# Optimization experiments

Measured on AMD Instinct MI355X. Metric: run time of the kernel, lower is better.

The kernel has to match this reference:

```python
import jax, jax.numpy as jnp
import numpy as np

H = 16      # num_heads
D = 1024    # hidden_dim
HD = D // H # head_dim = 64


def setup_inputs() -> dict:
    key = jax.random.key(0)
    ks = jax.random.split(key, 9)
    s = 1.0 / np.sqrt(D)
    return {
        "hidden_states": jax.random.normal(ks[0], (2, 2048, D), dtype=jnp.float32),
        "wq": jax.random.uniform(ks[1], (D, D), jnp.float32, -s, s),
        "bq": jax.random.uniform(ks[2], (D,), jnp.float32, -s, s),
        "wk": jax.random.uniform(ks[3], (D, D), jnp.float32, -s, s),
        "bk": jax.random.uniform(ks[4], (D,), jnp.float32, -s, s),
        "wv": jax.random.uniform(ks[5], (D, D), jnp.float32, -s, s),
        "bv": jax.random.uniform(ks[6], (D,), jnp.float32, -s, s),
        "wo": jax.random.uniform(ks[7], (D, D), jnp.float32, -s, s),
        "bo": jax.random.uniform(ks[8], (D,), jnp.float32, -s, s),
    }


def reference(hidden_states, wq, bq, wk, bk, wv, bv, wo, bo):
    B, L, _ = hidden_states.shape
    scale = HD ** -0.5
    # projections: [B,L,D] -> [B,H,L,HD]
    def split_heads(x):
        return x.reshape(B, L, H, HD).transpose(0, 2, 1, 3)
    q = split_heads(hidden_states @ wq.T + bq)
    k = split_heads(hidden_states @ wk.T + bk)
    v = split_heads(hidden_states @ wv.T + bv)
    # explicit [B,H,L,L] scores + softmax + weighted sum (faithful to source)
    scores = jnp.einsum("bhqd,bhkd->bhqk", q, k) * scale
    attn = jax.nn.softmax(scores, axis=-1)
    out = jnp.einsum("bhqk,bhkd->bhqd", attn, v)
    out = out.transpose(0, 2, 1, 3).reshape(B, L, D)
    return out @ wo.T + bo
```

## Files before the change

kernel.cpp:

```cpp
#include <hip/hip_runtime.h>
#include <math.h>

#define BATCH  2
#define SEQ    2048
#define NH     16
#define DMODEL 1024
#define DHEAD  64

typedef short short8 __attribute__((ext_vector_type(8)));
typedef float f32x4 __attribute__((ext_vector_type(4)));

#define QSCALE 0.18033688011112042f

__device__ __forceinline__ ushort f2bf(float f) {
  unsigned int u = __builtin_bit_cast(unsigned int, f);
  u = (u + 0x7FFFu + ((u >> 16) & 1u)) >> 16;
  return (ushort)u;
}

__global__ __launch_bounds__(256) void cast_all(
    const float* __restrict__ hs, const float* __restrict__ wq,
    const float* __restrict__ wk, const float* __restrict__ wv,
    const float* __restrict__ wo,
    ushort* __restrict__ hsb, ushort* __restrict__ wqb,
    ushort* __restrict__ wkb, ushort* __restrict__ wvb,
    ushort* __restrict__ wob) {
  const int z = blockIdx.y;
  const float* s = (z == 0) ? hs : (z == 1) ? wq : (z == 2) ? wk
                   : (z == 3) ? wv : wo;
  ushort* d = (z == 0) ? hsb : (z == 1) ? wqb : (z == 2) ? wkb
              : (z == 3) ? wvb : wob;
  const int n = (z == 0) ? BATCH * SEQ * DMODEL : DMODEL * DMODEL;
  const int i = (blockIdx.x * 256 + threadIdx.x) * 8;
  if (i < n) {
    const float4 a = *(const float4*)(s + i);
    const float4 b = *(const float4*)(s + i + 4);
    short8 o;
    o[0] = (short)f2bf(a.x); o[1] = (short)f2bf(a.y);
    o[2] = (short)f2bf(a.z); o[3] = (short)f2bf(a.w);
    o[4] = (short)f2bf(b.x); o[5] = (short)f2bf(b.y);
    o[6] = (short)f2bf(b.z); o[7] = (short)f2bf(b.w);
    *(short8*)(d + i) = o;
  }
}

__device__ __forceinline__ void mfma_gemm_core(
    const ushort* __restrict__ X, const ushort* __restrict__ W,
    f32x4 (&acc)[4][2]) {
  __shared__ ushort Al[128][40];
  __shared__ ushort Bl[128][40];
  const int tid = threadIdx.x;
  const int lane = tid & 63;
  const int w8 = tid >> 6;
  const int wm = w8 >> 2;
  const int wn = w8 & 3;
  const int m16 = lane & 15;
  const int g4 = lane >> 4;
  const int m0 = blockIdx.y << 7;
  const int n0 = blockIdx.x << 7;

  const int srow = tid >> 2;
  const int sseg = (tid & 3) << 3;
  const ushort* ap = X + (size_t)(m0 + srow) * DMODEL + sseg;
  const ushort* wp = W + (size_t)(n0 + srow) * DMODEL + sseg;

  short8 pa = *(const short8*)(ap);
  short8 pb = *(const short8*)(wp);

  for (int kt = 0; kt < DMODEL / 32; ++kt) {
    __syncthreads();
    *(short8*)&Al[srow][sseg] = pa;
    *(short8*)&Bl[srow][sseg] = pb;
    __syncthreads();
    if (kt < DMODEL / 32 - 1) {
      pa = *(const short8*)(ap + (kt + 1) * 32);
      pb = *(const short8*)(wp + (kt + 1) * 32);
    }
    short8 af[4], bf[2];
#pragma unroll
    for (int mi = 0; mi < 4; ++mi)
      af[mi] = *(const short8*)&Al[(wm << 6) + (mi << 4) + m16][g4 << 3];
#pragma unroll
    for (int ni = 0; ni < 2; ++ni)
      bf[ni] = *(const short8*)&Bl[(wn << 5) + (ni << 4) + m16][g4 << 3];
#pragma unroll
    for (int mi = 0; mi < 4; ++mi)
#pragma unroll
      for (int ni = 0; ni < 2; ++ni)
        acc[mi][ni] = __builtin_amdgcn_mfma_f32_16x16x32_bf16(
            af[mi], bf[ni], acc[mi][ni], 0, 0, 0);
  }
}

__global__ __launch_bounds__(512) void qkv_mfma(
    const ushort* __restrict__ X,
    const ushort* __restrict__ wqb, const ushort* __restrict__ wkb,
    const ushort* __restrict__ wvb,
    const float* __restrict__ bq, const float* __restrict__ bk,
    const float* __restrict__ bv,
    ushort* __restrict__ Qb, ushort* __restrict__ Kb,
    ushort* __restrict__ Vb) {
  const int z = blockIdx.z;
  const ushort* W = (z == 0) ? wqb : (z == 1) ? wkb : wvb;
  const float* bias = (z == 0) ? bq : (z == 1) ? bk : bv;
  ushort* Y = (z == 0) ? Qb : (z == 1) ? Kb : Vb;
  const float oscale = (z == 0) ? QSCALE : 1.0f;

  f32x4 acc[4][2];
#pragma unroll
  for (int mi = 0; mi < 4; ++mi)
#pragma unroll
    for (int ni = 0; ni < 2; ++ni) acc[mi][ni] = (f32x4){0.f, 0.f, 0.f, 0.f};
  mfma_gemm_core(X, W, acc);

  const int tid = threadIdx.x;
  const int lane = tid & 63;
  const int w8 = tid >> 6;
  const int wm = w8 >> 2, wn = w8 & 3;
  const int m16 = lane & 15, g4 = lane >> 4;
  const int m0 = blockIdx.y << 7, n0 = blockIdx.x << 7;
#pragma unroll
  for (int ni = 0; ni < 2; ++ni) {
    const int col = n0 + (wn << 5) + (ni << 4) + m16;
    const float bv4 = bias[col];
#pragma unroll
    for (int mi = 0; mi < 4; ++mi)
#pragma unroll
      for (int r = 0; r < 4; ++r) {
        const int row = m0 + (wm << 6) + (mi << 4) + (g4 << 2) + r;
        Y[(size_t)row * DMODEL + col] = f2bf((acc[mi][ni][r] + bv4) * oscale);
      }
  }
}

__global__ __launch_bounds__(512) void oproj_mfma(
    const ushort* __restrict__ X, const ushort* __restrict__ wob,
    const float* __restrict__ bo, float* __restrict__ Y) {
  f32x4 acc[4][2];
#pragma unroll
  for (int mi = 0; mi < 4; ++mi)
#pragma unroll
    for (int ni = 0; ni < 2; ++ni) acc[mi][ni] = (f32x4){0.f, 0.f, 0.f, 0.f};
  mfma_gemm_core(X, wob, acc);

  const int tid = threadIdx.x;
  const int lane = tid & 63;
  const int w8 = tid >> 6;
  const int wm = w8 >> 2, wn = w8 & 3;
  const int m16 = lane & 15, g4 = lane >> 4;
  const int m0 = blockIdx.y << 7, n0 = blockIdx.x << 7;
#pragma unroll
  for (int ni = 0; ni < 2; ++ni) {
    const int col = n0 + (wn << 5) + (ni << 4) + m16;
    const float bv4 = bo[col];
#pragma unroll
    for (int mi = 0; mi < 4; ++mi)
#pragma unroll
      for (int r = 0; r < 4; ++r) {
        const int row = m0 + (wm << 6) + (mi << 4) + (g4 << 2) + r;
        Y[(size_t)row * DMODEL + col] = acc[mi][ni][r] + bv4;
      }
  }
}

__global__ __launch_bounds__(512, 4) void attn_mfma(
    const ushort* __restrict__ Q, const ushort* __restrict__ K,
    const ushort* __restrict__ V, ushort* __restrict__ O) {
  __shared__ ushort Klds[2][64][72];
  __shared__ ushort Vlds[2][64][72];
  __shared__ ushort Plds[8][16][72];

  const int tid = threadIdx.x;
  const int lane = tid & 63;
  const int wv = tid >> 6;
  const int m16 = lane & 15;
  const int g4 = lane >> 4;
  const int b = blockIdx.z;
  const int h = blockIdx.y;
  const int q0 = (blockIdx.x << 7) + (wv << 4);

  const size_t base = ((size_t)b * SEQ) * DMODEL + h * DHEAD;

  short8 qf[2];
  {
    const ushort* qp = Q + base + (size_t)(q0 + m16) * DMODEL + (g4 << 3);
    qf[0] = *(const short8*)(qp);
    qf[1] = *(const short8*)(qp + 32);
  }

  f32x4 oacc[4];
#pragma unroll
  for (int dt = 0; dt < 4; ++dt) oacc[dt] = (f32x4){0.f, 0.f, 0.f, 0.f};
  float mrow = -1e30f;
  float lsum = 0.f;

  const int skey = tid >> 3;
  const int sseg = tid & 7;
  const ushort* kgp = K + base + (size_t)skey * DMODEL + (sseg << 3);
  const ushort* vgp = V + base + (size_t)skey * DMODEL + (sseg << 3);
  const int vswz_key = skey ^ (sseg << 3);

  short8 kvec = *(const short8*)(kgp);
  short8 vvec = *(const short8*)(vgp);

  int p = 0;
  for (int kt = 0; kt < SEQ / 64; ++kt) {
    *(short8*)&Klds[p][skey][sseg << 3] = kvec;
#pragma unroll
    for (int i = 0; i < 8; ++i)
      Vlds[p][(sseg << 3) + i][vswz_key] = ((const ushort*)&vvec)[i];
    __syncthreads();
    if (kt + 1 < SEQ / 64) {
      const size_t koff = (size_t)(kt + 1) * 64 * DMODEL;
      kvec = *(const short8*)(kgp + koff);
      vvec = *(const short8*)(vgp + koff);
    }

    f32x4 s[4];
#pragma unroll
    for (int kt2 = 0; kt2 < 4; ++kt2) s[kt2] = (f32x4){0.f, 0.f, 0.f, 0.f};
    __builtin_amdgcn_s_setprio(1);
#pragma unroll
    for (int ks = 0; ks < 2; ++ks) {
#pragma unroll
      for (int kt2 = 0; kt2 < 4; ++kt2) {
        const short8 kf =
            *(const short8*)&Klds[p][(kt2 << 4) + m16][(ks << 5) + (g4 << 3)];
        s[kt2] =
            __builtin_amdgcn_mfma_f32_16x16x32_bf16(kf, qf[ks], s[kt2], 0, 0, 0);
      }
    }
    __builtin_amdgcn_s_setprio(0);

    float t01 = fmaxf(fmaxf(s[0][0], s[0][1]), fmaxf(s[0][2], s[0][3]));
    float t11 = fmaxf(fmaxf(s[1][0], s[1][1]), fmaxf(s[1][2], s[1][3]));
    float t21 = fmaxf(fmaxf(s[2][0], s[2][1]), fmaxf(s[2][2], s[2][3]));
    float t31 = fmaxf(fmaxf(s[3][0], s[3][1]), fmaxf(s[3][2], s[3][3]));
    float tred = fmaxf(fmaxf(t01, t11), fmaxf(t21, t31));
    tred = fmaxf(tred, __shfl_xor(tred, 16));
    tred = fmaxf(tred, __shfl_xor(tred, 32));
    if (!__all(tred <= mrow + 8.0f)) {
      const float mnew = fmaxf(mrow, tred);
      const float corr = exp2f(mrow - mnew);
      lsum *= corr;
      const float cb0 = __shfl(corr, (g4 << 2) + 0);
      const float cb1 = __shfl(corr, (g4 << 2) + 1);
      const float cb2 = __shfl(corr, (g4 << 2) + 2);
      const float cb3 = __shfl(corr, (g4 << 2) + 3);
#pragma unroll
      for (int dt = 0; dt < 4; ++dt) {
        oacc[dt][0] *= cb0; oacc[dt][1] *= cb1;
        oacc[dt][2] *= cb2; oacc[dt][3] *= cb3;
      }
      mrow = mnew;
    }
    float ps = 0.f;
#pragma unroll
    for (int kt2 = 0; kt2 < 4; ++kt2)
#pragma unroll
      for (int r = 0; r < 4; ++r) {
        const float pv = exp2f(s[kt2][r] - mrow);
        s[kt2][r] = pv;
        ps += pv;
      }
    lsum += ps;

#pragma unroll
    for (int kt2 = 0; kt2 < 4; ++kt2) {
      const uint lo = (uint)f2bf(s[kt2][0]) | ((uint)f2bf(s[kt2][1]) << 16);
      const uint hi = (uint)f2bf(s[kt2][2]) | ((uint)f2bf(s[kt2][3]) << 16);
      uint2* dst = (uint2*)&Plds[wv][m16][(kt2 << 4) + (g4 << 2)];
      *dst = make_uint2(lo, hi);
    }

    short8 pf[2];
#pragma unroll
    for (int ks = 0; ks < 2; ++ks)
      pf[ks] = *(const short8*)&Plds[wv][m16][(ks << 5) + (g4 << 3)];
    __builtin_amdgcn_s_setprio(1);
#pragma unroll
    for (int dt = 0; dt < 4; ++dt) {
      const int d = (dt << 4) + m16;
      const int swz = (d >> 3) << 3;
#pragma unroll
      for (int ks = 0; ks < 2; ++ks) {
        const short8 vf =
            *(const short8*)&Vlds[p][d][((ks << 5) + (g4 << 3)) ^ swz];
        oacc[dt] =
            __builtin_amdgcn_mfma_f32_16x16x32_bf16(pf[ks], vf, oacc[dt], 0, 0, 0);
      }
    }
    __builtin_amdgcn_s_setprio(0);
    p ^= 1;
  }

  lsum += __shfl_xor(lsum, 16);
  lsum += __shfl_xor(lsum, 32);
  const float inv = 1.0f / lsum;
  const float inv0 = __shfl(inv, (g4 << 2) + 0);
  const float inv1 = __shfl(inv, (g4 << 2) + 1);
  const float inv2 = __shfl(inv, (g4 << 2) + 2);
  const float inv3 = __shfl(inv, (g4 << 2) + 3);
  const float invr[4] = {inv0, inv1, inv2, inv3};
#pragma unroll
  for (int r = 0; r < 4; ++r) {
    const size_t row = (size_t)(q0 + (g4 << 2) + r);
    ushort* op = O + ((size_t)b * SEQ + row) * DMODEL + h * DHEAD + m16;
#pragma unroll
    for (int dt = 0; dt < 4; ++dt) op[dt << 4] = f2bf(oacc[dt][r] * invr[r]);
  }
}

extern "C" void kernel_launch(void* const* d_in, const int* in_sizes, int n_in,
                              void* d_out, int out_size, void* d_ws,
                              size_t ws_size, hipStream_t stream) {
  const float* hs = (const float*)d_in[0];
  const float* wq = (const float*)d_in[1];
  const float* bq = (const float*)d_in[2];
  const float* wk = (const float*)d_in[3];
  const float* bk = (const float*)d_in[4];
  const float* wv = (const float*)d_in[5];
  const float* bv = (const float*)d_in[6];
  const float* wo = (const float*)d_in[7];
  const float* bo = (const float*)d_in[8];
  float* out = (float*)d_out;

  const size_t elems = (size_t)BATCH * SEQ * DMODEL;
  const size_t welems = (size_t)DMODEL * DMODEL;
  ushort* hsb = (ushort*)d_ws;
  ushort* wqb = hsb + elems;
  ushort* wkb = wqb + welems;
  ushort* wvb = wkb + welems;
  ushort* wob = wvb + welems;
  ushort* Qb = wob + welems;
  ushort* Kb = Qb + elems;
  ushort* Vb = Kb + elems;
  ushort* Ab = Vb + elems;

  cast_all<<<dim3((int)(elems / (256 * 8)), 5, 1), 256, 0, stream>>>(
      hs, wq, wk, wv, wo, hsb, wqb, wkb, wvb, wob);
  qkv_mfma<<<dim3(DMODEL / 128, (BATCH * SEQ) / 128, 3), 512, 0, stream>>>(
      hsb, wqb, wkb, wvb, bq, bk, bv, Qb, Kb, Vb);
  attn_mfma<<<dim3(SEQ / 128, NH, BATCH), 512, 0, stream>>>(Qb, Kb, Vb, Ab);
  oproj_mfma<<<dim3(DMODEL / 128, (BATCH * SEQ) / 128, 1), 512, 0, stream>>>(
      Ab, wob, bo, out);
}
```

Before: 146.9 us.

## Process 32 query rows per wave in attention and use packed bf16 convert

The attention kernel now runs 4 waves per block instead of 8, and each wave handles two 16-row query tiles. Each K and V fragment read from LDS is reused for two MFMAs, which halves LDS fragment traffic per unit of work. Each thread now stages two K/V segments per tile. The P-to-bf16 conversion uses the hardware v_cvt_pk_bf16_f32 instruction instead of manual rounding. The costs are higher register pressure and fewer waves per block, which may reduce latency hiding.

```diff
diff --git a/kernel.cpp b/kernel.cpp
--- a/kernel.cpp
+++ b/kernel.cpp
@@ -16,6 +16,12 @@
   unsigned int u = __builtin_bit_cast(unsigned int, f);
   u = (u + 0x7FFFu + ((u >> 16) & 1u)) >> 16;
   return (ushort)u;
+}
+
+__device__ __forceinline__ unsigned int cvtpk(float lo, float hi) {
+  unsigned int r;
+  asm("v_cvt_pk_bf16_f32 %0, %1, %2" : "=v"(r) : "v"(lo), "v"(hi));
+  return r;
 }
 
 __global__ __launch_bounds__(256) void cast_all(
@@ -163,12 +169,12 @@
   }
 }
 
-__global__ __launch_bounds__(512, 4) void attn_mfma(
+__global__ __launch_bounds__(256, 2) void attn_mfma(
     const ushort* __restrict__ Q, const ushort* __restrict__ K,
     const ushort* __restrict__ V, ushort* __restrict__ O) {
   __shared__ ushort Klds[2][64][72];
   __shared__ ushort Vlds[2][64][72];
-  __shared__ ushort Plds[8][16][72];
+  __shared__ ushort Plds[4][32][72];
 
   const int tid = threadIdx.x;
   const int lane = tid & 63;
@@ -177,48 +183,62 @@
   const int g4 = lane >> 4;
   const int b = blockIdx.z;
   const int h = blockIdx.y;
-  const int q0 = (blockIdx.x << 7) + (wv << 4);
+  const int q0 = (blockIdx.x << 7) + (wv << 5);
 
   const size_t base = ((size_t)b * SEQ) * DMODEL + h * DHEAD;
 
-  short8 qf[2];
-  {
-    const ushort* qp = Q + base + (size_t)(q0 + m16) * DMODEL + (g4 << 3);
-    qf[0] = *(const short8*)(qp);
-    qf[1] = *(const short8*)(qp + 32);
-  }
-
-  f32x4 oacc[4];
-#pragma unroll
-  for (int dt = 0; dt < 4; ++dt) oacc[dt] = (f32x4){0.f, 0.f, 0.f, 0.f};
-  float mrow = -1e30f;
-  float lsum = 0.f;
-
-  const int skey = tid >> 3;
-  const int sseg = tid & 7;
-  const ushort* kgp = K + base + (size_t)skey * DMODEL + (sseg << 3);
-  const ushort* vgp = V + base + (size_t)skey * DMODEL + (sseg << 3);
-  const int vswz_key = skey ^ (sseg << 3);
-
-  short8 kvec = *(const short8*)(kgp);
-  short8 vvec = *(const short8*)(vgp);
+  short8 qf[2][2];
+#pragma unroll
+  for (int qh = 0; qh < 2; ++qh) {
+    const ushort* qp =
+        Q + base + (size_t)(q0 + (qh << 4) + m16) * DMODEL + (g4 << 3);
+    qf[qh][0] = *(const short8*)(qp);
+    qf[qh][1] = *(const short8*)(qp + 32);
+  }
+
+  f32x4 oacc[2][4];
+#pragma unroll
+  for (int qh = 0; qh < 2; ++qh)
+#pragma unroll
+    for (int dt = 0; dt < 4; ++dt) oacc[qh][dt] = (f32x4){0.f, 0.f, 0.f, 0.f};
+  float mrow[2] = {-1e30f, -1e30f};
+  float lsum[2] = {0.f, 0.f};
+
+  const int skey = tid >> 2;
+  const int sb = tid & 3;
+  const ushort* kgp = K + base + (size_t)skey * DMODEL + (sb << 3);
+  const ushort* vgp = V + base + (size_t)skey * DMODEL + (sb << 3);
+  const int vsw0 = skey ^ (sb << 3);
+  const int vsw1 = skey ^ ((sb + 4) << 3);
+
+  short8 kv0 = *(const short8*)(kgp);
+  short8 kv1 = *(const short8*)(kgp + 32);
+  short8 vv0 = *(const short8*)(vgp);
+  short8 vv1 = *(const short8*)(vgp + 32);
 
   int p = 0;
   for (int kt = 0; kt < SEQ / 64; ++kt) {
-    *(short8*)&Klds[p][skey][sseg << 3] = kvec;
-#pragma unroll
-    for (int i = 0; i < 8; ++i)
-      Vlds[p][(sseg << 3) + i][vswz_key] = ((const ushort*)&vvec)[i];
+    *(short8*)&Klds[p][skey][sb << 3] = kv0;
+    *(short8*)&Klds[p][skey][(sb + 4) << 3] = kv1;
+#pragma unroll
+    for (int i = 0; i < 8; ++i) {
+      Vlds[p][(sb << 3) + i][vsw0] = ((const ushort*)&vv0)[i];
+      Vlds[p][((sb + 4) << 3) + i][vsw1] = ((const ushort*)&vv1)[i];
+    }
     __syncthreads();
     if (kt + 1 < SEQ / 64) {
       const size_t koff = (size_t)(kt + 1) * 64 * DMODEL;
-      kvec = *(const short8*)(kgp + koff);
-      vvec = *(const short8*)(vgp + koff);
-    }
-
-    f32x4 s[4];
-#pragma unroll
-    for (int kt2 = 0; kt2 < 4; ++kt2) s[kt2] = (f32x4){0.f, 0.f, 0.f, 0.f};
+      kv0 = *(const short8*)(kgp + koff);
+      kv1 = *(const short8*)(kgp + koff + 32);
+      vv0 = *(const short8*)(vgp + koff);
+      vv1 = *(const short8*)(vgp + koff + 32);
+    }
+
+    f32x4 s[2][4];
+#pragma unroll
+    for (int qh = 0; qh < 2; ++qh)
+#pragma unroll
+      for (int kt2 = 0; kt2 < 4; ++kt2) s[qh][kt2] = (f32x4){0.f, 0.f, 0.f, 0.f};
     __builtin_amdgcn_s_setprio(1);
 #pragma unroll
     for (int ks = 0; ks < 2; ++ks) {
@@ -226,57 +246,69 @@
       for (int kt2 = 0; kt2 < 4; ++kt2) {
         const short8 kf =
             *(const short8*)&Klds[p][(kt2 << 4) + m16][(ks << 5) + (g4 << 3)];
-        s[kt2] =
-            __builtin_amdgcn_mfma_f32_16x16x32_bf16(kf, qf[ks], s[kt2], 0, 0, 0);
+        s[0][kt2] =
+            __builtin_amdgcn_mfma_f32_16x16x32_bf16(kf, qf[0][ks], s[0][kt2], 0, 0, 0);
+        s[1][kt2] =
+            __builtin_amdgcn_mfma_f32_16x16x32_bf16(kf, qf[1][ks], s[1][kt2], 0, 0, 0);
       }
     }
     __builtin_amdgcn_s_setprio(0);
 
-    float t01 = fmaxf(fmaxf(s[0][0], s[0][1]), fmaxf(s[0][2], s[0][3]));
-    float t11 = fmaxf(fmaxf(s[1][0], s[1][1]), fmaxf(s[1][2], s[1][3]));
-    float t21 = fmaxf(fmaxf(s[2][0], s[2][1]), fmaxf(s[2][2], s[2][3]));
-    float t31 = fmaxf(fmaxf(s[3][0], s[3][1]), fmaxf(s[3][2], s[3][3]));
-    float tred = fmaxf(fmaxf(t01, t11), fmaxf(t21, t31));
-    tred = fmaxf(tred, __shfl_xor(tred, 16));
-    tred = fmaxf(tred, __shfl_xor(tred, 32));
-    if (!__all(tred <= mrow + 8.0f)) {
-      const float mnew = fmaxf(mrow, tred);
-      const float corr = exp2f(mrow - mnew);
-      lsum *= corr;
-      const float cb0 = __shfl(corr, (g4 << 2) + 0);
-      const float cb1 = __shfl(corr, (g4 << 2) + 1);
-      const float cb2 = __shfl(corr, (g4 << 2) + 2);
-      const float cb3 = __shfl(corr, (g4 << 2) + 3);
-#pragma unroll
-      for (int dt = 0; dt < 4; ++dt) {
-        oacc[dt][0] *= cb0; oacc[dt][1] *= cb1;
-        oacc[dt][2] *= cb2; oacc[dt][3] *= cb3;
-      }
-      mrow = mnew;
-    }
-    float ps = 0.f;
-#pragma unroll
-    for (int kt2 = 0; kt2 < 4; ++kt2)
-#pragma unroll
-      for (int r = 0; r < 4; ++r) {
-        const float pv = exp2f(s[kt2][r] - mrow);
-        s[kt2][r] = pv;
-        ps += pv;
-      }
-    lsum += ps;
-
-#pragma unroll
-    for (int kt2 = 0; kt2 < 4; ++kt2) {
-      const uint lo = (uint)f2bf(s[kt2][0]) | ((uint)f2bf(s[kt2][1]) << 16);
-      const uint hi = (uint)f2bf(s[kt2][2]) | ((uint)f2bf(s[kt2][3]) << 16);
-      uint2* dst = (uint2*)&Plds[wv][m16][(kt2 << 4) + (g4 << 2)];
-      *dst = make_uint2(lo, hi);
-    }
-
-    short8 pf[2];
-#pragma unroll
-    for (int ks = 0; ks < 2; ++ks)
-      pf[ks] = *(const short8*)&Plds[wv][m16][(ks << 5) + (g4 << 3)];
+#pragma unroll
+    for (int qh = 0; qh < 2; ++qh) {
+      float t0 = fmaxf(fmaxf(s[qh][0][0], s[qh][0][1]),
+                       fmaxf(s[qh][0][2], s[qh][0][3]));
+      float t1 = fmaxf(fmaxf(s[qh][1][0], s[qh][1][1]),
+                       fmaxf(s[qh][1][2], s[qh][1][3]));
+      float t2 = fmaxf(fmaxf(s[qh][2][0], s[qh][2][1]),
+                       fmaxf(s[qh][2][2], s[qh][2][3]));
+      float t3 = fmaxf(fmaxf(s[qh][3][0], s[qh][3][1]),
+                       fmaxf(s[qh][3][2], s[qh][3][3]));
+      float tred = fmaxf(fmaxf(t0, t1), fmaxf(t2, t3));
+      tred = fmaxf(tred, __shfl_xor(tred, 16));
+      tred = fmaxf(tred, __shfl_xor(tred, 32));
+      if (!__all(tred <= mrow[qh] + 8.0f)) {
+        const float mnew = fmaxf(mrow[qh], tred);
+        const float corr = exp2f(mrow[qh] - mnew);
+        lsum[qh] *= corr;
+        const float cb0 = __shfl(corr, (g4 << 2) + 0);
+        const float cb1 = __shfl(corr, (g4 << 2) + 1);
+        const float cb2 = __shfl(corr, (g4 << 2) + 2);
+        const float cb3 = __shfl(corr, (g4 << 2) + 3);
+#pragma unroll
+        for (int dt = 0; dt < 4; ++dt) {
+          oacc[qh][dt][0] *= cb0; oacc[qh][dt][1] *= cb1;
+          oacc[qh][dt][2] *= cb2; oacc[qh][dt][3] *= cb3;
+        }
+        mrow[qh] = mnew;
+      }
+      float ps = 0.f;
+#pragma unroll
+      for (int kt2 = 0; kt2 < 4; ++kt2)
+#pragma unroll
+        for (int r = 0; r < 4; ++r) {
+          const float pv = exp2f(s[qh][kt2][r] - mrow[qh]);
+          s[qh][kt2][r] = pv;
+          ps += pv;
+        }
+      lsum[qh] += ps;
+#pragma unroll
+      for (int kt2 = 0; kt2 < 4; ++kt2) {
+        const unsigned int lo = cvtpk(s[qh][kt2][0], s[qh][kt2][1]);
+        const unsigned int hi = cvtpk(s[qh][kt2][2], s[qh][kt2][3]);
+        uint2* dst =
+            (uint2*)&Plds[wv][(qh << 4) + m16][(kt2 << 4) + (g4 << 2)];
+        *dst = make_uint2(lo, hi);
+      }
+    }
+
+    short8 pf[2][2];
+#pragma unroll
+    for (int qh = 0; qh < 2; ++qh)
+#pragma unroll
+      for (int ks = 0; ks < 2; ++ks)
+        pf[qh][ks] =
+            *(const short8*)&Plds[wv][(qh << 4) + m16][(ks << 5) + (g4 << 3)];
     __builtin_amdgcn_s_setprio(1);
 #pragma unroll
     for (int dt = 0; dt < 4; ++dt) {
@@ -286,28 +318,35 @@
       for (int ks = 0; ks < 2; ++ks) {
         const short8 vf =
             *(const short8*)&Vlds[p][d][((ks << 5) + (g4 << 3)) ^ swz];
-        oacc[dt] =
-            __builtin_amdgcn_mfma_f32_16x16x32_bf16(pf[ks], vf, oacc[dt], 0, 0, 0);
+        oacc[0][dt] =
+            __builtin_amdgcn_mfma_f32_16x16x32_bf16(pf[0][ks], vf, oacc[0][dt], 0, 0, 0);
+        oacc[1][dt] =
+            __builtin_amdgcn_mfma_f32_16x16x32_bf16(pf[1][ks], vf, oacc[1][dt], 0, 0, 0);
       }
     }
     __builtin_amdgcn_s_setprio(0);
     p ^= 1;
   }
 
-  lsum += __shfl_xor(lsum, 16);
-  lsum += __shfl_xor(lsum, 32);
-  const float inv = 1.0f / lsum;
-  const float inv0 = __shfl(inv, (g4 << 2) + 0);
-  const float inv1 = __shfl(inv, (g4 << 2) + 1);
-  const float inv2 = __shfl(inv, (g4 << 2) + 2);
-  const float inv3 = __shfl(inv, (g4 << 2) + 3);
-  const float invr[4] = {inv0, inv1, inv2, inv3};
-#pragma unroll
-  for (int r = 0; r < 4; ++r) {
-    const size_t row = (size_t)(q0 + (g4 << 2) + r);
-    ushort* op = O + ((size_t)b * SEQ + row) * DMODEL + h * DHEAD + m16;
-#pragma unroll
-    for (int dt = 0; dt < 4; ++dt) op[dt << 4] = f2bf(oacc[dt][r] * invr[r]);
+#pragma unroll
+  for (int qh = 0; qh < 2; ++qh) {
+    float ls = lsum[qh];
+    ls += __shfl_xor(ls, 16);
+    ls += __shfl_xor(ls, 32);
+    const float inv = 1.0f / ls;
+    const float inv0 = __shfl(inv, (g4 << 2) + 0);
+    const float inv1 = __shfl(inv, (g4 << 2) + 1);
+    const float inv2 = __shfl(inv, (g4 << 2) + 2);
+    const float inv3 = __shfl(inv, (g4 << 2) + 3);
+    const float invr[4] = {inv0, inv1, inv2, inv3};
+#pragma unroll
+    for (int r = 0; r < 4; ++r) {
+      const size_t row = (size_t)(q0 + (qh << 4) + (g4 << 2) + r);
+      ushort* op = O + ((size_t)b * SEQ + row) * DMODEL + h * DHEAD + m16;
+#pragma unroll
+      for (int dt = 0; dt < 4; ++dt)
+        op[dt << 4] = f2bf(oacc[qh][dt][r] * invr[r]);
+    }
   }
 }
 
@@ -341,7 +380,7 @@
       hs, wq, wk, wv, wo, hsb, wqb, wkb, wvb, wob);
   qkv_mfma<<<dim3(DMODEL / 128, (BATCH * SEQ) / 128, 3), 512, 0, stream>>>(
       hsb, wqb, wkb, wvb, bq, bk, bv, Qb, Kb, Vb);
-  attn_mfma<<<dim3(SEQ / 128, NH, BATCH), 512, 0, stream>>>(Qb, Kb, Vb, Ab);
+  attn_mfma<<<dim3(SEQ / 128, NH, BATCH), 256, 0, stream>>>(Qb, Kb, Vb, Ab);
   oproj_mfma<<<dim3(DMODEL / 128, (BATCH * SEQ) / 128, 1), 512, 0, stream>>>(
       Ab, wob, bo, out);
 }
```

Result: no change. 148.2 us (+0.9%).

## Transpose attention probabilities in registers and halve attention block size

Applied to the files above, without the earlier changes.

The softmax probabilities are now packed with the hardware v_cvt_pk_bf16_f32 instruction and rearranged into the MFMA A-operand layout with cross-lane shuffles. This replaces the per-wave LDS round trip (Plds write then read), which is removed. The attention kernel also moves from 512-thread blocks covering 128 queries to 256-thread blocks covering 64 queries, so each thread loads two K/V vectors per tile. The grid doubles, which may raise occupancy and cut LDS use, but each key tile is now loaded more often across blocks.

```diff
diff --git a/kernel.cpp b/kernel.cpp
--- a/kernel.cpp
+++ b/kernel.cpp
@@ -16,6 +16,12 @@
   unsigned int u = __builtin_bit_cast(unsigned int, f);
   u = (u + 0x7FFFu + ((u >> 16) & 1u)) >> 16;
   return (ushort)u;
+}
+
+__device__ __forceinline__ unsigned int cvtpk(float lo, float hi) {
+  unsigned int r;
+  asm("v_cvt_pk_bf16_f32 %0, %1, %2" : "=v"(r) : "v"(lo), "v"(hi));
+  return r;
 }
 
 __global__ __launch_bounds__(256) void cast_all(
@@ -163,12 +169,19 @@
   }
 }
 
-__global__ __launch_bounds__(512, 4) void attn_mfma(
+#define SWAPSTEP(Wa, Wb, dist, hi)                  \
+  {                                                 \
+    const unsigned int gv = (hi) ? (Wa) : (Wb);     \
+    const unsigned int gt = __shfl_xor(gv, (dist)); \
+    (Wa) = (hi) ? gt : (Wa);                        \
+    (Wb) = (hi) ? (Wb) : gt;                        \
+  }
+
+__global__ __launch_bounds__(256, 4) void attn_mfma(
     const ushort* __restrict__ Q, const ushort* __restrict__ K,
     const ushort* __restrict__ V, ushort* __restrict__ O) {
   __shared__ ushort Klds[2][64][72];
   __shared__ ushort Vlds[2][64][72];
-  __shared__ ushort Plds[8][16][72];
 
   const int tid = threadIdx.x;
   const int lane = tid & 63;
@@ -177,7 +190,7 @@
   const int g4 = lane >> 4;
   const int b = blockIdx.z;
   const int h = blockIdx.y;
-  const int q0 = (blockIdx.x << 7) + (wv << 4);
+  const int q0 = (blockIdx.x << 6) + (wv << 4);
 
   const size_t base = ((size_t)b * SEQ) * DMODEL + h * DHEAD;
 
@@ -194,26 +207,34 @@
   float mrow = -1e30f;
   float lsum = 0.f;
 
-  const int skey = tid >> 3;
-  const int sseg = tid & 7;
-  const ushort* kgp = K + base + (size_t)skey * DMODEL + (sseg << 3);
-  const ushort* vgp = V + base + (size_t)skey * DMODEL + (sseg << 3);
-  const int vswz_key = skey ^ (sseg << 3);
-
-  short8 kvec = *(const short8*)(kgp);
-  short8 vvec = *(const short8*)(vgp);
+  const int skey = tid >> 2;
+  const int sb = tid & 3;
+  const ushort* kgp = K + base + (size_t)skey * DMODEL + (sb << 3);
+  const ushort* vgp = V + base + (size_t)skey * DMODEL + (sb << 3);
+  const int vsw0 = skey ^ (sb << 3);
+  const int vsw1 = skey ^ ((sb + 4) << 3);
+
+  short8 kv0 = *(const short8*)(kgp);
+  short8 kv1 = *(const short8*)(kgp + 32);
+  short8 vv0 = *(const short8*)(vgp);
+  short8 vv1 = *(const short8*)(vgp + 32);
 
   int p = 0;
   for (int kt = 0; kt < SEQ / 64; ++kt) {
-    *(short8*)&Klds[p][skey][sseg << 3] = kvec;
-#pragma unroll
-    for (int i = 0; i < 8; ++i)
-      Vlds[p][(sseg << 3) + i][vswz_key] = ((const ushort*)&vvec)[i];
+    *(short8*)&Klds[p][skey][sb << 3] = kv0;
+    *(short8*)&Klds[p][skey][(sb + 4) << 3] = kv1;
+#pragma unroll
+    for (int i = 0; i < 8; ++i) {
+      Vlds[p][(sb << 3) + i][vsw0] = ((const ushort*)&vv0)[i];
+      Vlds[p][((sb + 4) << 3) + i][vsw1] = ((const ushort*)&vv1)[i];
+    }
     __syncthreads();
     if (kt + 1 < SEQ / 64) {
       const size_t koff = (size_t)(kt + 1) * 64 * DMODEL;
-      kvec = *(const short8*)(kgp + koff);
-      vvec = *(const short8*)(vgp + koff);
+      kv0 = *(const short8*)(kgp + koff);
+      kv1 = *(const short8*)(kgp + koff + 32);
+      vv0 = *(const short8*)(vgp + koff);
+      vv1 = *(const short8*)(vgp + koff + 32);
     }
 
     f32x4 s[4];
@@ -232,11 +253,11 @@
     }
     __builtin_amdgcn_s_setprio(0);
 
-    float t01 = fmaxf(fmaxf(s[0][0], s[0][1]), fmaxf(s[0][2], s[0][3]));
-    float t11 = fmaxf(fmaxf(s[1][0], s[1][1]), fmaxf(s[1][2], s[1][3]));
-    float t21 = fmaxf(fmaxf(s[2][0], s[2][1]), fmaxf(s[2][2], s[2][3]));
-    float t31 = fmaxf(fmaxf(s[3][0], s[3][1]), fmaxf(s[3][2], s[3][3]));
-    float tred = fmaxf(fmaxf(t01, t11), fmaxf(t21, t31));
+    float t0 = fmaxf(fmaxf(s[0][0], s[0][1]), fmaxf(s[0][2], s[0][3]));
+    float t1 = fmaxf(fmaxf(s[1][0], s[1][1]), fmaxf(s[1][2], s[1][3]));
+    float t2 = fmaxf(fmaxf(s[2][0], s[2][1]), fmaxf(s[2][2], s[2][3]));
+    float t3 = fmaxf(fmaxf(s[3][0], s[3][1]), fmaxf(s[3][2], s[3][3]));
+    float tred = fmaxf(fmaxf(t0, t1), fmaxf(t2, t3));
     tred = fmaxf(tred, __shfl_xor(tred, 16));
     tred = fmaxf(tred, __shfl_xor(tred, 32));
     if (!__all(tred <= mrow + 8.0f)) {
@@ -265,30 +286,45 @@
       }
     lsum += ps;
 
-#pragma unroll
-    for (int kt2 = 0; kt2 < 4; ++kt2) {
-      const uint lo = (uint)f2bf(s[kt2][0]) | ((uint)f2bf(s[kt2][1]) << 16);
-      const uint hi = (uint)f2bf(s[kt2][2]) | ((uint)f2bf(s[kt2][3]) << 16);
-      uint2* dst = (uint2*)&Plds[wv][m16][(kt2 << 4) + (g4 << 2)];
-      *dst = make_uint2(lo, hi);
-    }
-
-    short8 pf[2];
-#pragma unroll
-    for (int ks = 0; ks < 2; ++ks)
-      pf[ks] = *(const short8*)&Plds[wv][m16][(ks << 5) + (g4 << 3)];
+    unsigned int W0 = cvtpk(s[0][0], s[0][1]);
+    unsigned int W1 = cvtpk(s[0][2], s[0][3]);
+    unsigned int W2 = cvtpk(s[1][0], s[1][1]);
+    unsigned int W3 = cvtpk(s[1][2], s[1][3]);
+    unsigned int W4 = cvtpk(s[2][0], s[2][1]);
+    unsigned int W5 = cvtpk(s[2][2], s[2][3]);
+    unsigned int W6 = cvtpk(s[3][0], s[3][1]);
+    unsigned int W7 = cvtpk(s[3][2], s[3][3]);
+    {
+      const bool hi = (lane & 32) != 0;
+      SWAPSTEP(W0, W2, 32, hi);
+      SWAPSTEP(W1, W3, 32, hi);
+      SWAPSTEP(W4, W6, 32, hi);
+      SWAPSTEP(W5, W7, 32, hi);
+    }
+    {
+      const bool hi = (lane & 16) != 0;
+      SWAPSTEP(W0, W2, 16, hi);
+      SWAPSTEP(W1, W3, 16, hi);
+      SWAPSTEP(W4, W6, 16, hi);
+      SWAPSTEP(W5, W7, 16, hi);
+    }
+    union { unsigned int u[4]; short8 v; } pk0, pk1;
+    pk0.u[0] = W0; pk0.u[1] = W1; pk0.u[2] = W2; pk0.u[3] = W3;
+    pk1.u[0] = W4; pk1.u[1] = W5; pk1.u[2] = W6; pk1.u[3] = W7;
+
     __builtin_amdgcn_s_setprio(1);
 #pragma unroll
     for (int dt = 0; dt < 4; ++dt) {
       const int d = (dt << 4) + m16;
       const int swz = (d >> 3) << 3;
-#pragma unroll
-      for (int ks = 0; ks < 2; ++ks) {
-        const short8 vf =
-            *(const short8*)&Vlds[p][d][((ks << 5) + (g4 << 3)) ^ swz];
-        oacc[dt] =
-            __builtin_amdgcn_mfma_f32_16x16x32_bf16(pf[ks], vf, oacc[dt], 0, 0, 0);
-      }
+      const short8 vf0 =
+          *(const short8*)&Vlds[p][d][((g4 << 3)) ^ swz];
+      oacc[dt] =
+          __builtin_amdgcn_mfma_f32_16x16x32_bf16(pk0.v, vf0, oacc[dt], 0, 0, 0);
+      const short8 vf1 =
+          *(const short8*)&Vlds[p][d][(32 + (g4 << 3)) ^ swz];
+      oacc[dt] =
+          __builtin_amdgcn_mfma_f32_16x16x32_bf16(pk1.v, vf1, oacc[dt], 0, 0, 0);
     }
     __builtin_amdgcn_s_setprio(0);
     p ^= 1;
@@ -341,7 +377,7 @@
       hs, wq, wk, wv, wo, hsb, wqb, wkb, wvb, wob);
   qkv_mfma<<<dim3(DMODEL / 128, (BATCH * SEQ) / 128, 3), 512, 0, stream>>>(
       hsb, wqb, wkb, wvb, bq, bk, bv, Qb, Kb, Vb);
-  attn_mfma<<<dim3(SEQ / 128, NH, BATCH), 512, 0, stream>>>(Qb, Kb, Vb, Ab);
+  attn_mfma<<<dim3(SEQ / 64, NH, BATCH), 256, 0, stream>>>(Qb, Kb, Vb, Ab);
   oproj_mfma<<<dim3(DMODEL / 128, (BATCH * SEQ) / 128, 1), 512, 0, stream>>>(
       Ab, wob, bo, out);
 }
```

Measured after the change: 155.0 us. +5.5%, slower.
